# Kernel tuning notes

Measured on AMD Instinct MI355X. Metric: run time of the kernel, lower is better.

The kernel has to match this reference:

```python
import jax, jax.numpy as jnp
import numpy as np

V, S, D, C = 400000, 4096, 300, 4  # vocab, seq_len, embed_dim, act classes


def setup_inputs() -> dict:
    key = jax.random.key(0)
    ks = jax.random.split(key, 6)
    sc = 1.0 / np.sqrt(D)
    return {
        "x_batch": jax.random.randint(ks[0], (1, S), 0, V),
        "emb_table": jax.random.normal(ks[1], (V, D), jnp.float32) * 0.02,
        "W1": jax.random.normal(ks[2], (D, D), jnp.float32) * sc,
        "b1": jnp.zeros((D,), jnp.float32),
        "Wb": jax.random.normal(ks[3], (D, D), jnp.float32) * sc,  # Bilinear weight [1,D,D] squeezed
        "bb": jnp.zeros((1,), jnp.float32),                        # Bilinear bias
        "W2": jax.random.normal(ks[4], (C, D), jnp.float32) * sc,
        "b2": jnp.zeros((C,), jnp.float32),
    }


def reference(x_batch, emb_table, W1, b1, Wb, bb, W2, b2):
    embed = emb_table[x_batch]                  # [1, S, D] embedding lookup
    dense = embed.mean(axis=1)                  # [1, D] mean pooling
    mid = dense @ W1.T + b1                     # [1, D] hidden layer (dropout = identity in eval)
    # per-token bilinear attention scores: a_s = e_s^T Wb mid + bb (vectorized over s)
    scores = jnp.einsum('sd,de,e->s', embed[0], Wb, mid[0])[None, :] + bb  # [1, S]
    reward = jax.nn.softmax(scores, axis=1)     # [1, S]
    addition = jnp.mean(reward[:, :, None] * embed, axis=1)  # [1, D] weighted mean pooling
    output = (mid + addition) @ W2.T + b2       # [1, C]
    return output, reward
```

## Files before the change

kernel.cpp:

```cpp
#include <hip/hip_runtime.h>
#include <hip/hip_cooperative_groups.h>
#include <math.h>

namespace cg = cooperative_groups;

#define SEQ  4096
#define DIM  300
#define NCLS 4
#define NB   128

#define OFF_P1   0
#define OFF_MID  (OFF_P1 + NB * DIM)
#define OFF_U    (OFF_MID + DIM)
#define OFF_SC   (OFF_U + DIM)
#define OFF_BMAX (OFF_SC + SEQ)
#define OFF_P2   (OFF_BMAX + NB)

__global__ __launch_bounds__(256) void fused_dan(
        const int* __restrict__ x, const float* __restrict__ emb,
        const float* __restrict__ W1, const float* __restrict__ b1,
        const float* __restrict__ Wb, const float* __restrict__ bb,
        const float* __restrict__ W2, const float* __restrict__ b2,
        float* __restrict__ out, float* __restrict__ ws) {
    cg::grid_group grid = cg::this_grid();

    float* P1     = ws + OFF_P1;
    float* MID    = ws + OFF_MID;
    float* U      = ws + OFF_U;
    float* SC     = ws + OFF_SC;
    float* BMAX   = ws + OFF_BMAX;
    float* P2     = ws + OFF_P2;
    float* reward = out + NCLS;

    __shared__ float lds[4][320];
    __shared__ float vec[DIM];
    __shared__ float red[4];

    const int wave = threadIdx.x >> 6, lane = threadIdx.x & 63;
    const int bid  = blockIdx.x;
    const int s0   = bid * 32 + wave * 8;

    {
        float a0 = 0.f, a1 = 0.f, a2 = 0.f, a3 = 0.f, a4 = 0.f;
        #pragma unroll
        for (int r = 0; r < 8; ++r) {
            const float* row = emb + (size_t)x[s0 + r] * DIM;
            a0 += row[lane];
            a1 += row[lane + 64];
            a2 += row[lane + 128];
            a3 += row[lane + 192];
            if (lane < DIM - 256) a4 += row[lane + 256];
        }
        lds[wave][lane]       = a0;
        lds[wave][lane + 64]  = a1;
        lds[wave][lane + 128] = a2;
        lds[wave][lane + 192] = a3;
        lds[wave][lane + 256] = a4;
        __syncthreads();
        for (int d = threadIdx.x; d < DIM; d += 256)
            P1[bid * DIM + d] = lds[0][d] + lds[1][d] + lds[2][d] + lds[3][d];
    }
    grid.sync();

    if (bid < 75) {
        for (int d = threadIdx.x; d < DIM; d += 256) {
            float s = 0.f;
            for (int b = 0; b < NB; ++b) s += P1[b * DIM + d];
            vec[d] = s * (1.0f / (float)SEQ);
        }
        __syncthreads();
        const int i    = bid * 4 + wave;
        const float* w = W1 + (size_t)i * DIM;
        float s = w[lane] * vec[lane] + w[lane + 64] * vec[lane + 64]
                + w[lane + 128] * vec[lane + 128]
                + w[lane + 192] * vec[lane + 192];
        if (lane < DIM - 256) s += w[lane + 256] * vec[lane + 256];
        for (int off = 32; off; off >>= 1) s += __shfl_down(s, off);
        if (lane == 0) MID[i] = s + b1[i];
    }
    grid.sync();

    if (bid < 75) {
        for (int d = threadIdx.x; d < DIM; d += 256) vec[d] = MID[d];
        __syncthreads();
        const int i    = bid * 4 + wave;
        const float* w = Wb + (size_t)i * DIM;
        float s = w[lane] * vec[lane] + w[lane + 64] * vec[lane + 64]
                + w[lane + 128] * vec[lane + 128]
                + w[lane + 192] * vec[lane + 192];
        if (lane < DIM - 256) s += w[lane + 256] * vec[lane + 256];
        for (int off = 32; off; off >>= 1) s += __shfl_down(s, off);
        if (lane == 0) U[i] = s;
    }
    grid.sync();

    {
        const float u0 = U[lane], u1 = U[lane + 64], u2 = U[lane + 128],
                    u3 = U[lane + 192];
        const float u4  = (lane < DIM - 256) ? U[lane + 256] : 0.f;
        const float bbv = bb[0];
        float wmax = -1e30f;
        #pragma unroll
        for (int r = 0; r < 8; ++r) {
            const float* row = emb + (size_t)x[s0 + r] * DIM;
            float s = row[lane] * u0 + row[lane + 64] * u1
                    + row[lane + 128] * u2 + row[lane + 192] * u3;
            if (lane < DIM - 256) s += row[lane + 256] * u4;
            for (int off = 32; off; off >>= 1) s += __shfl_down(s, off);
            if (lane == 0) {
                s += bbv;
                SC[s0 + r] = s;
                wmax = fmaxf(wmax, s);
            }
        }
        if (lane == 0) red[wave] = wmax;
        __syncthreads();
        if (threadIdx.x == 0)
            BMAX[bid] =
                fmaxf(fmaxf(red[0], red[1]), fmaxf(red[2], red[3]));
    }
    grid.sync();

    {
        float m = -1e30f;
        for (int i = threadIdx.x; i < NB; i += 256) m = fmaxf(m, BMAX[i]);
        for (int off = 32; off; off >>= 1) m = fmaxf(m, __shfl_down(m, off));
        if (lane == 0) red[wave] = m;
        __syncthreads();
        const float mx = fmaxf(fmaxf(red[0], red[1]), fmaxf(red[2], red[3]));
        __syncthreads();
        float s = 0.f;
        for (int i = threadIdx.x; i < SEQ; i += 256) s += expf(SC[i] - mx);
        for (int off = 32; off; off >>= 1) s += __shfl_down(s, off);
        if (lane == 0) red[wave] = s;
        __syncthreads();
        const float inv = 1.0f / (red[0] + red[1] + red[2] + red[3]);

        float a0 = 0.f, a1 = 0.f, a2 = 0.f, a3 = 0.f, a4 = 0.f;
        #pragma unroll
        for (int r = 0; r < 8; ++r) {
            const int srow = s0 + r;
            const float rw = expf(SC[srow] - mx) * inv;
            if (lane == 0) reward[srow] = rw;
            const float* row = emb + (size_t)x[srow] * DIM;
            a0 += rw * row[lane];
            a1 += rw * row[lane + 64];
            a2 += rw * row[lane + 128];
            a3 += rw * row[lane + 192];
            if (lane < DIM - 256) a4 += rw * row[lane + 256];
        }
        lds[wave][lane]       = a0;
        lds[wave][lane + 64]  = a1;
        lds[wave][lane + 128] = a2;
        lds[wave][lane + 192] = a3;
        lds[wave][lane + 256] = a4;
        __syncthreads();
        for (int d = threadIdx.x; d < DIM; d += 256)
            P2[bid * DIM + d] = lds[0][d] + lds[1][d] + lds[2][d] + lds[3][d];
    }
    grid.sync();

    if (bid == 0) {
        for (int d = threadIdx.x; d < DIM; d += 256) {
            float s = 0.f;
            for (int b = 0; b < NB; ++b) s += P2[b * DIM + d];
            vec[d] = MID[d] + s * (1.0f / (float)SEQ);
        }
        __syncthreads();
        const float* w = W2 + (size_t)wave * DIM;
        float s = w[lane] * vec[lane] + w[lane + 64] * vec[lane + 64]
                + w[lane + 128] * vec[lane + 128]
                + w[lane + 192] * vec[lane + 192];
        if (lane < DIM - 256) s += w[lane + 256] * vec[lane + 256];
        for (int off = 32; off; off >>= 1) s += __shfl_down(s, off);
        if (lane == 0) out[wave] = s + b2[wave];
    }
}

extern "C" void kernel_launch(void* const* d_in, const int* in_sizes, int n_in,
                              void* d_out, int out_size, void* d_ws,
                              size_t ws_size, hipStream_t stream) {
    const int*   x   = (const int*)d_in[0];
    const float* emb = (const float*)d_in[1];
    const float* W1  = (const float*)d_in[2];
    const float* b1  = (const float*)d_in[3];
    const float* Wb  = (const float*)d_in[4];
    const float* bb  = (const float*)d_in[5];
    const float* W2  = (const float*)d_in[6];
    const float* b2  = (const float*)d_in[7];
    float* out = (float*)d_out;
    float* ws  = (float*)d_ws;

    void* args[] = {(void*)&x,  (void*)&emb, (void*)&W1, (void*)&b1,
                    (void*)&Wb, (void*)&bb,  (void*)&W2, (void*)&b2,
                    (void*)&out, (void*)&ws};
    hipLaunchCooperativeKernel((void*)fused_dan, dim3(NB), dim3(256), args, 0,
                               stream);
}
```

Measured before the change: 651.4 us.

## Replace cooperative grid syncs with three kernels and max-free softmax

Drops the single cooperative kernel with five grid.sync barriers and splits the work into three ordinary launches. Each block of the middle kernel computes mid redundantly, which merges two grid-wide phases. Scoring and weighted pooling happen in one pass over the embeddings, with the softmax done without subtracting the max. A last-block atomic counter then does the normalization and the final W2 product. Loads use float4. Skipping the max subtraction can overflow expf for large scores, and the last block serially rescales all rewards.

```diff
diff --git a/kernel.cpp b/kernel.cpp
--- a/kernel.cpp
+++ b/kernel.cpp
@@ -1,180 +1,198 @@
 #include <hip/hip_runtime.h>
-#include <hip/hip_cooperative_groups.h>
 #include <math.h>
-
-namespace cg = cooperative_groups;
 
 #define SEQ  4096
 #define DIM  300
 #define NCLS 4
 #define NB   128
+#define NCH  75
+#define INV_S (1.0f / 4096.0f)
 
 #define OFF_P1   0
 #define OFF_MID  (OFF_P1 + NB * DIM)
 #define OFF_U    (OFF_MID + DIM)
-#define OFF_SC   (OFF_U + DIM)
-#define OFF_BMAX (OFF_SC + SEQ)
-#define OFF_P2   (OFF_BMAX + NB)
-
-__global__ __launch_bounds__(256) void fused_dan(
+#define OFF_P2   (OFF_U + DIM)
+#define OFF_ZP   (OFF_P2 + NB * DIM)
+#define OFF_CNT  (OFF_ZP + NB)
+
+__device__ __forceinline__ float dot4(float4 a, float4 b) {
+    return a.x * b.x + a.y * b.y + a.z * b.z + a.w * b.w;
+}
+
+__global__ __launch_bounds__(256) void k_gather_sum(
         const int* __restrict__ x, const float* __restrict__ emb,
+        float* __restrict__ ws) {
+    float* P1 = ws + OFF_P1;
+    if (blockIdx.x == 0 && threadIdx.x == 0) *(int*)(ws + OFF_CNT) = 0;
+    __shared__ float4 lds4[4][80];
+    const int wave = threadIdx.x >> 6, lane = threadIdx.x & 63;
+    float4 aa = {0.f, 0.f, 0.f, 0.f}, ab = {0.f, 0.f, 0.f, 0.f};
+    const int s0 = blockIdx.x * 32 + wave * 8;
+    #pragma unroll
+    for (int r = 0; r < 8; ++r) {
+        const float4* row = (const float4*)(emb + (size_t)x[s0 + r] * DIM);
+        float4 ra = row[lane];
+        aa.x += ra.x; aa.y += ra.y; aa.z += ra.z; aa.w += ra.w;
+        if (lane < NCH - 64) {
+            float4 rb = row[64 + lane];
+            ab.x += rb.x; ab.y += rb.y; ab.z += rb.z; ab.w += rb.w;
+        }
+    }
+    lds4[wave][lane] = aa;
+    if (lane < NCH - 64) lds4[wave][64 + lane] = ab;
+    __syncthreads();
+    for (int c = threadIdx.x; c < NCH; c += 256) {
+        float4 a = lds4[0][c], b = lds4[1][c], d = lds4[2][c], e = lds4[3][c];
+        float4 v;
+        v.x = a.x + b.x + d.x + e.x;
+        v.y = a.y + b.y + d.y + e.y;
+        v.z = a.z + b.z + d.z + e.z;
+        v.w = a.w + b.w + d.w + e.w;
+        ((float4*)P1)[blockIdx.x * NCH + c] = v;
+    }
+}
+
+__global__ __launch_bounds__(256) void k_mid_u(
         const float* __restrict__ W1, const float* __restrict__ b1,
-        const float* __restrict__ Wb, const float* __restrict__ bb,
-        const float* __restrict__ W2, const float* __restrict__ b2,
-        float* __restrict__ out, float* __restrict__ ws) {
-    cg::grid_group grid = cg::this_grid();
-
-    float* P1     = ws + OFF_P1;
-    float* MID    = ws + OFF_MID;
-    float* U      = ws + OFF_U;
-    float* SC     = ws + OFF_SC;
-    float* BMAX   = ws + OFF_BMAX;
-    float* P2     = ws + OFF_P2;
+        const float* __restrict__ Wb, float* __restrict__ ws) {
+    const float* P1 = ws + OFF_P1;
+    float* MID = ws + OFF_MID;
+    float* U   = ws + OFF_U;
+    __shared__ float vec[304];
+    __shared__ float midv[304];
+    const int tid = threadIdx.x;
+
+    for (int c = tid; c < NCH; c += 256) {
+        float4 s = {0.f, 0.f, 0.f, 0.f};
+        const float4* p = (const float4*)P1;
+        for (int b = 0; b < NB; ++b) {
+            float4 t = p[b * NCH + c];
+            s.x += t.x; s.y += t.y; s.z += t.z; s.w += t.w;
+        }
+        float4 v = {s.x * INV_S, s.y * INV_S, s.z * INV_S, s.w * INV_S};
+        ((float4*)vec)[c] = v;
+    }
+    __syncthreads();
+
+    for (int i = tid; i < DIM; i += 256) {
+        const float4* w = (const float4*)(W1 + (size_t)i * DIM);
+        float m = 0.f;
+        for (int c = 0; c < NCH; ++c) m += dot4(w[c], ((float4*)vec)[c]);
+        midv[i] = m + b1[i];
+    }
+    __syncthreads();
+
+    if (blockIdx.x == 0)
+        for (int c = tid; c < NCH; c += 256)
+            ((float4*)MID)[c] = ((float4*)midv)[c];
+
+    const int wave = tid >> 6, lane = tid & 63;
+    const int i = blockIdx.x * 4 + wave;
+    const float4* w  = (const float4*)(Wb + (size_t)i * DIM);
+    const float4* mv = (const float4*)midv;
+    float s = dot4(w[lane], mv[lane]);
+    if (lane < NCH - 64) s += dot4(w[64 + lane], mv[64 + lane]);
+    for (int off = 32; off; off >>= 1) s += __shfl_down(s, off);
+    if (lane == 0) U[i] = s;
+}
+
+__global__ __launch_bounds__(256) void k_score_pool(
+        const int* __restrict__ x, const float* __restrict__ emb,
+        const float* __restrict__ bb, const float* __restrict__ W2,
+        const float* __restrict__ b2, float* __restrict__ out,
+        float* __restrict__ ws) {
+    const float* MID = ws + OFF_MID;
+    const float* U   = ws + OFF_U;
+    float* P2  = ws + OFF_P2;
+    float* ZP  = ws + OFF_ZP;
+    int*   cnt = (int*)(ws + OFF_CNT);
     float* reward = out + NCLS;
 
-    __shared__ float lds[4][320];
-    __shared__ float vec[DIM];
+    __shared__ float4 lds4[4][80];
     __shared__ float red[4];
+    __shared__ float vecE[304];
+    __shared__ int last;
 
     const int wave = threadIdx.x >> 6, lane = threadIdx.x & 63;
-    const int bid  = blockIdx.x;
-    const int s0   = bid * 32 + wave * 8;
-
-    {
-        float a0 = 0.f, a1 = 0.f, a2 = 0.f, a3 = 0.f, a4 = 0.f;
-        #pragma unroll
-        for (int r = 0; r < 8; ++r) {
-            const float* row = emb + (size_t)x[s0 + r] * DIM;
-            a0 += row[lane];
-            a1 += row[lane + 64];
-            a2 += row[lane + 128];
-            a3 += row[lane + 192];
-            if (lane < DIM - 256) a4 += row[lane + 256];
+    const float4* U4 = (const float4*)U;
+    const float4 ua = U4[lane];
+    const float4 ub = (lane < NCH - 64) ? U4[64 + lane]
+                                        : make_float4(0.f, 0.f, 0.f, 0.f);
+    const float bbv = bb[0];
+
+    float4 aa = {0.f, 0.f, 0.f, 0.f}, ab = {0.f, 0.f, 0.f, 0.f};
+    float zp = 0.f;
+    const int s0 = blockIdx.x * 32 + wave * 8;
+    #pragma unroll
+    for (int r = 0; r < 8; ++r) {
+        const int srow = s0 + r;
+        const float4* row = (const float4*)(emb + (size_t)x[srow] * DIM);
+        const float4 ra = row[lane];
+        const float4 rb = (lane < NCH - 64) ? row[64 + lane]
+                                            : make_float4(0.f, 0.f, 0.f, 0.f);
+        float s = dot4(ra, ua) + dot4(rb, ub);
+        for (int off = 32; off; off >>= 1) s += __shfl_down(s, off);
+        s = __shfl(s, 0);
+        const float w = expf(s + bbv);
+        if (lane == 0) reward[srow] = w;
+        zp += w;
+        aa.x += w * ra.x; aa.y += w * ra.y; aa.z += w * ra.z; aa.w += w * ra.w;
+        ab.x += w * rb.x; ab.y += w * rb.y; ab.z += w * rb.z; ab.w += w * rb.w;
+    }
+    lds4[wave][lane] = aa;
+    if (lane < NCH - 64) lds4[wave][64 + lane] = ab;
+    if (lane == 0) red[wave] = zp;
+    __syncthreads();
+    for (int c = threadIdx.x; c < NCH; c += 256) {
+        float4 a = lds4[0][c], b = lds4[1][c], d = lds4[2][c], e = lds4[3][c];
+        float4 v;
+        v.x = a.x + b.x + d.x + e.x;
+        v.y = a.y + b.y + d.y + e.y;
+        v.z = a.z + b.z + d.z + e.z;
+        v.w = a.w + b.w + d.w + e.w;
+        ((float4*)P2)[blockIdx.x * NCH + c] = v;
+    }
+    if (threadIdx.x == 0)
+        ZP[blockIdx.x] = red[0] + red[1] + red[2] + red[3];
+
+    __threadfence();
+    __syncthreads();
+    if (threadIdx.x == 0) last = (atomicAdd(cnt, 1) == NB - 1);
+    __syncthreads();
+    if (!last) return;
+    __threadfence();
+
+    float z = 0.f;
+    for (int i = threadIdx.x; i < NB; i += 256) z += ZP[i];
+    for (int off = 32; off; off >>= 1) z += __shfl_down(z, off);
+    if (lane == 0) red[wave] = z;
+    __syncthreads();
+    const float Z = red[0] + red[1] + red[2] + red[3];
+    const float invZ = 1.0f / Z;
+
+    for (int i = threadIdx.x; i < SEQ; i += 256) reward[i] *= invZ;
+
+    const float scale = invZ * INV_S;
+    for (int c = threadIdx.x; c < NCH; c += 256) {
+        float4 s = {0.f, 0.f, 0.f, 0.f};
+        const float4* p = (const float4*)P2;
+        for (int b = 0; b < NB; ++b) {
+            float4 t = p[b * NCH + c];
+            s.x += t.x; s.y += t.y; s.z += t.z; s.w += t.w;
         }
-        lds[wave][lane]       = a0;
-        lds[wave][lane + 64]  = a1;
-        lds[wave][lane + 128] = a2;
-        lds[wave][lane + 192] = a3;
-        lds[wave][lane + 256] = a4;
-        __syncthreads();
-        for (int d = threadIdx.x; d < DIM; d += 256)
-            P1[bid * DIM + d] = lds[0][d] + lds[1][d] + lds[2][d] + lds[3][d];
-    }
-    grid.sync();
-
-    if (bid < 75) {
-        for (int d = threadIdx.x; d < DIM; d += 256) {
-            float s = 0.f;
-            for (int b = 0; b < NB; ++b) s += P1[b * DIM + d];
-            vec[d] = s * (1.0f / (float)SEQ);
-        }
-        __syncthreads();
-        const int i    = bid * 4 + wave;
-        const float* w = W1 + (size_t)i * DIM;
-        float s = w[lane] * vec[lane] + w[lane + 64] * vec[lane + 64]
-                + w[lane + 128] * vec[lane + 128]
-                + w[lane + 192] * vec[lane + 192];
-        if (lane < DIM - 256) s += w[lane + 256] * vec[lane + 256];
-        for (int off = 32; off; off >>= 1) s += __shfl_down(s, off);
-        if (lane == 0) MID[i] = s + b1[i];
-    }
-    grid.sync();
-
-    if (bid < 75) {
-        for (int d = threadIdx.x; d < DIM; d += 256) vec[d] = MID[d];
-        __syncthreads();
-        const int i    = bid * 4 + wave;
-        const float* w = Wb + (size_t)i * DIM;
-        float s = w[lane] * vec[lane] + w[lane + 64] * vec[lane + 64]
-                + w[lane + 128] * vec[lane + 128]
-                + w[lane + 192] * vec[lane + 192];
-        if (lane < DIM - 256) s += w[lane + 256] * vec[lane + 256];
-        for (int off = 32; off; off >>= 1) s += __shfl_down(s, off);
-        if (lane == 0) U[i] = s;
-    }
-    grid.sync();
-
-    {
-        const float u0 = U[lane], u1 = U[lane + 64], u2 = U[lane + 128],
-                    u3 = U[lane + 192];
-        const float u4  = (lane < DIM - 256) ? U[lane + 256] : 0.f;
-        const float bbv = bb[0];
-        float wmax = -1e30f;
-        #pragma unroll
-        for (int r = 0; r < 8; ++r) {
-            const float* row = emb + (size_t)x[s0 + r] * DIM;
-            float s = row[lane] * u0 + row[lane + 64] * u1
-                    + row[lane + 128] * u2 + row[lane + 192] * u3;
-            if (lane < DIM - 256) s += row[lane + 256] * u4;
-            for (int off = 32; off; off >>= 1) s += __shfl_down(s, off);
-            if (lane == 0) {
-                s += bbv;
-                SC[s0 + r] = s;
-                wmax = fmaxf(wmax, s);
-            }
-        }
-        if (lane == 0) red[wave] = wmax;
-        __syncthreads();
-        if (threadIdx.x == 0)
-            BMAX[bid] =
-                fmaxf(fmaxf(red[0], red[1]), fmaxf(red[2], red[3]));
-    }
-    grid.sync();
-
-    {
-        float m = -1e30f;
-        for (int i = threadIdx.x; i < NB; i += 256) m = fmaxf(m, BMAX[i]);
-        for (int off = 32; off; off >>= 1) m = fmaxf(m, __shfl_down(m, off));
-        if (lane == 0) red[wave] = m;
-        __syncthreads();
-        const float mx = fmaxf(fmaxf(red[0], red[1]), fmaxf(red[2], red[3]));
-        __syncthreads();
-        float s = 0.f;
-        for (int i = threadIdx.x; i < SEQ; i += 256) s += expf(SC[i] - mx);
-        for (int off = 32; off; off >>= 1) s += __shfl_down(s, off);
-        if (lane == 0) red[wave] = s;
-        __syncthreads();
-        const float inv = 1.0f / (red[0] + red[1] + red[2] + red[3]);
-
-        float a0 = 0.f, a1 = 0.f, a2 = 0.f, a3 = 0.f, a4 = 0.f;
-        #pragma unroll
-        for (int r = 0; r < 8; ++r) {
-            const int srow = s0 + r;
-            const float rw = expf(SC[srow] - mx) * inv;
-            if (lane == 0) reward[srow] = rw;
-            const float* row = emb + (size_t)x[srow] * DIM;
-            a0 += rw * row[lane];
-            a1 += rw * row[lane + 64];
-            a2 += rw * row[lane + 128];
-            a3 += rw * row[lane + 192];
-            if (lane < DIM - 256) a4 += rw * row[lane + 256];
-        }
-        lds[wave][lane]       = a0;
-        lds[wave][lane + 64]  = a1;
-        lds[wave][lane + 128] = a2;
-        lds[wave][lane + 192] = a3;
-        lds[wave][lane + 256] = a4;
-        __syncthreads();
-        for (int d = threadIdx.x; d < DIM; d += 256)
-            P2[bid * DIM + d] = lds[0][d] + lds[1][d] + lds[2][d] + lds[3][d];
-    }
-    grid.sync();
-
-    if (bid == 0) {
-        for (int d = threadIdx.x; d < DIM; d += 256) {
-            float s = 0.f;
-            for (int b = 0; b < NB; ++b) s += P2[b * DIM + d];
-            vec[d] = MID[d] + s * (1.0f / (float)SEQ);
-        }
-        __syncthreads();
-        const float* w = W2 + (size_t)wave * DIM;
-        float s = w[lane] * vec[lane] + w[lane + 64] * vec[lane + 64]
-                + w[lane + 128] * vec[lane + 128]
-                + w[lane + 192] * vec[lane + 192];
-        if (lane < DIM - 256) s += w[lane + 256] * vec[lane + 256];
-        for (int off = 32; off; off >>= 1) s += __shfl_down(s, off);
-        if (lane == 0) out[wave] = s + b2[wave];
-    }
+        float4 m = ((const float4*)MID)[c];
+        float4 v = {m.x + s.x * scale, m.y + s.y * scale,
+                    m.z + s.z * scale, m.w + s.w * scale};
+        ((float4*)vecE)[c] = v;
+    }
+    __syncthreads();
+
+    const float4* w  = (const float4*)(W2 + (size_t)wave * DIM);
+    const float4* ve = (const float4*)vecE;
+    float s = dot4(w[lane], ve[lane]);
+    if (lane < NCH - 64) s += dot4(w[64 + lane], ve[64 + lane]);
+    for (int off = 32; off; off >>= 1) s += __shfl_down(s, off);
+    if (lane == 0) out[wave] = s + b2[wave];
 }
 
 extern "C" void kernel_launch(void* const* d_in, const int* in_sizes, int n_in,
@@ -191,9 +209,7 @@
     float* out = (float*)d_out;
     float* ws  = (float*)d_ws;
 
-    void* args[] = {(void*)&x,  (void*)&emb, (void*)&W1, (void*)&b1,
-                    (void*)&Wb, (void*)&bb,  (void*)&W2, (void*)&b2,
-                    (void*)&out, (void*)&ws};
-    hipLaunchCooperativeKernel((void*)fused_dan, dim3(NB), dim3(256), args, 0,
-                               stream);
-}
+    k_gather_sum<<<NB, 256, 0, stream>>>(x, emb, ws);
+    k_mid_u<<<75, 256, 0, stream>>>(W1, b1, Wb, ws);
+    k_score_pool<<<NB, 256, 0, stream>>>(x, emb, bb, W2, b2, out, ws);
+}
```

New measurement: 576.4 us. -11.5%, faster.
